# Kernel optimization log

Hardware: AMD Instinct MI355X
Metric: run time of the kernel (lower is better)

## Reference

```python
import jax, jax.numpy as jnp
import numpy as np
import math

D = 2048
H = 16
DH = D // H
DFF = 8192
B = 4
S = 2048
EPS = 1e-12


def gelu(x):
    # faithful tanh-approx gelu from source
    return 0.5 * x * (1.0 + jnp.tanh(math.sqrt(2.0 / math.pi) * (x + 0.044715 * x ** 3)))


def global_layernorm(x, w, b):
    # torch.mean(x)/torch.var(x): scalar mean and UNBIASED variance over ALL elements
    mean = jnp.mean(x)
    var = jnp.var(x, ddof=1)
    return (x - mean) / jnp.sqrt(var + EPS) * w + b


def setup_inputs() -> dict:
    key = jax.random.key(0)
    ks = jax.random.split(key, 12)
    sd = 0.02
    return {
        "x": jax.random.normal(ks[0], (B, S, D), jnp.float32),
        "W1_w": jax.random.normal(ks[1], (3 * D, D), jnp.float32) * sd,
        "W1_b": jnp.zeros((3 * D,), jnp.float32),
        "W2_w": jax.random.normal(ks[2], (D, D), jnp.float32) * sd,
        "W2_b": jnp.zeros((D,), jnp.float32),
        "fc_w": jax.random.normal(ks[3], (DFF, D), jnp.float32) * sd,
        "fc_b": jnp.zeros((DFF,), jnp.float32),
        "proj_w": jax.random.normal(ks[4], (D, DFF), jnp.float32) * sd,
        "proj_b": jnp.zeros((D,), jnp.float32),
        "ln1_w": jnp.ones((D,), jnp.float32),
        "ln1_b": jnp.zeros((D,), jnp.float32),
        "ln2_w": jnp.ones((D,), jnp.float32),
        "ln2_b": jnp.zeros((D,), jnp.float32),
    }


def attn(x, W1_w, W1_b, W2_w, W2_b):
    X = x @ W1_w.T + W1_b                     # [B,S,3D]
    Q, K, V = jnp.split(X, 3, axis=2)         # each [B,S,D]
    # reshape(): view (B,S,H,Dh) then permute
    q = Q.reshape(B, S, H, DH).transpose(0, 2, 3, 1)  # [B,H,Dh,S]
    k = K.reshape(B, S, H, DH).transpose(0, 2, 1, 3)  # [B,H,S,Dh]
    v = V.reshape(B, S, H, DH).transpose(0, 2, 3, 1)  # [B,H,Dh,S]
    # heads(): scores over head-feature dim, scaled by sqrt(q.size(-1)) = sqrt(S)
    w = jnp.einsum('bhds,bhse->bhde', q, k) / math.sqrt(S)  # [B,H,Dh,Dh]
    w = jax.nn.softmax(w, axis=-1)
    out = jnp.einsum('bhde,bhes->bhds', w, v)  # [B,H,Dh,S]
    # cat(): raw contiguous view [B,H,Dh,S] -> [B,S,H*Dh] (memory-order reshape)
    out = out.reshape(B, S, H * DH)
    return out @ W2_w.T + W2_b


def ffn(x, fc_w, fc_b, proj_w, proj_b):
    h = gelu(x @ fc_w.T + fc_b)
    return h @ proj_w.T + proj_b


def reference(x, W1_w, W1_b, W2_w, W2_b, fc_w, fc_b, proj_w, proj_b,
              ln1_w, ln1_b, ln2_w, ln2_b):
    a = attn(x, W1_w, W1_b, W2_w, W2_b)
    x = global_layernorm(a + x, ln1_w, ln1_b)
    m = ffn(x, fc_w, fc_b, proj_w, proj_b)
    x = global_layernorm(m + x, ln2_w, ln2_b)
    return x
```

## Files before the change

kernel.cpp:

```cpp
#include <hip/hip_runtime.h>
#include <math.h>

typedef float floatx4 __attribute__((ext_vector_type(4)));
typedef __bf16 bf16x8 __attribute__((ext_vector_type(8)));
typedef unsigned short ushortx8 __attribute__((ext_vector_type(8)));
typedef unsigned short ushortx4 __attribute__((ext_vector_type(4)));
typedef unsigned short ushortx2 __attribute__((ext_vector_type(2)));

typedef unsigned int __attribute__((address_space(1))) as1_uint;
typedef unsigned int __attribute__((address_space(3))) as3_uint;

#define DEV static __device__ __forceinline__

DEV unsigned short f32_bf16(float f) {
  unsigned u = __float_as_uint(f);
  u += 0x7FFFu + ((u >> 16) & 1u);
  return (unsigned short)(u >> 16);
}
DEV float bf16_f32(unsigned short h) { return __uint_as_float(((unsigned)h) << 16); }
DEV float gelu_f(float x) {
  float t2 = 1.5957691216057308f * (x + 0.044715f * x * x * x);
  return x * __builtin_amdgcn_rcpf(1.0f + __expf(-t2));
}
DEV void gload16(const void* g, void* l) {
  __builtin_amdgcn_global_load_lds((const as1_uint*)g, (as3_uint*)l, 16, 0, 0);
}
DEV floatx4 mfma16(ushortx8 a, ushortx8 b, floatx4 c) {
  return __builtin_amdgcn_mfma_f32_16x16x32_bf16(
      __builtin_bit_cast(bf16x8, a), __builtin_bit_cast(bf16x8, b), c, 0, 0, 0);
}


__global__ void zero_f(float* p, int n) {
  int i = threadIdx.x;
  if (i < n) p[i] = 0.f;
}

__global__ void cvt_f32_bf16(const float* __restrict__ in, unsigned short* __restrict__ out,
                             long n4) {
  long i = (long)blockIdx.x * blockDim.x + threadIdx.x;
  if (i >= n4) return;
  float4 v = ((const float4*)in)[i];
  ushortx4 o;
  o.x = f32_bf16(v.x); o.y = f32_bf16(v.y); o.z = f32_bf16(v.z); o.w = f32_bf16(v.w);
  ((ushortx4*)out)[i] = o;
}

__global__ void cvt_cols(const float* __restrict__ in, unsigned short* __restrict__ out,
                         int cbase, int cwlog4, long n4) {
  long i = (long)blockIdx.x * blockDim.x + threadIdx.x;
  if (i >= n4) return;
  int n = (int)(i >> cwlog4);
  int k4 = (int)(i & ((1 << cwlog4) - 1)) << 2;
  float4 v = *(const float4*)&in[(size_t)n * 8192 + cbase + k4];
  ushortx4 o;
  o.x = f32_bf16(v.x); o.y = f32_bf16(v.y); o.z = f32_bf16(v.z); o.w = f32_bf16(v.w);
  *(ushortx4*)&out[((size_t)n << (cwlog4 + 2)) + k4] = o;
}

__global__ __launch_bounds__(256) void softmax_k(const float* __restrict__ sc,
                                                 unsigned short* __restrict__ probs) {
  int r = blockIdx.x * 4 + (threadIdx.x >> 6);
  int lane = threadIdx.x & 63;
  size_t base = (size_t)(r >> 7) * 16384 + (size_t)(r & 127) * 128 + lane * 2;
  float2 p0 = *(const float2*)&sc[base];
  float2 p1 = *(const float2*)&sc[base + 1048576];
  float2 p2 = *(const float2*)&sc[base + 2097152];
  float2 p3 = *(const float2*)&sc[base + 3145728];
  const float scale = 0.022097086912079608f;
  float vx = (p0.x + p1.x + p2.x + p3.x) * scale;
  float vy = (p0.y + p1.y + p2.y + p3.y) * scale;
  float m = fmaxf(vx, vy);
#pragma unroll
  for (int off = 32; off; off >>= 1) m = fmaxf(m, __shfl_xor(m, off));
  float ex = expf(vx - m), ey = expf(vy - m);
  float s = ex + ey;
#pragma unroll
  for (int off = 32; off; off >>= 1) s += __shfl_xor(s, off);
  float inv = 1.f / s;
  ushortx2 o;
  o.x = f32_bf16(ex * inv);
  o.y = f32_bf16(ey * inv);
  *(ushortx2*)&probs[base] = o;
}

__global__ void ln_apply(const float* __restrict__ r, const float* __restrict__ stats,
                         const float* __restrict__ w, const float* __restrict__ bia,
                         float* __restrict__ outF, unsigned short* __restrict__ outB, long n4) {
  long i = (long)blockIdx.x * blockDim.x + threadIdx.x;
  if (i >= n4) return;
  const double total = 16777216.0;
  double mean = (double)stats[0] / total;
  double var = ((double)stats[1] - total * mean * mean) / (total - 1.0);
  float rstd = (float)(1.0 / sqrt(var + 1e-12));
  float fm = (float)mean;
  int col = (int)((i * 4) & 2047);
  float4 v = ((const float4*)r)[i];
  float4 wv = *(const float4*)&w[col];
  float4 bv = *(const float4*)&bia[col];
  float4 o;
  o.x = (v.x - fm) * rstd * wv.x + bv.x;
  o.y = (v.y - fm) * rstd * wv.y + bv.y;
  o.z = (v.z - fm) * rstd * wv.z + bv.z;
  o.w = (v.w - fm) * rstd * wv.w + bv.w;
  if (outF) ((float4*)outF)[i] = o;
  if (outB) {
    ushortx4 ob;
    ob.x = f32_bf16(o.x); ob.y = f32_bf16(o.y); ob.z = f32_bf16(o.z); ob.w = f32_bf16(o.w);
    ((ushortx4*)outB)[i] = ob;
  }
}

__global__ __launch_bounds__(256) void gemm_bt(
    const unsigned short* __restrict__ A, int lda, long sAo, long sAi,
    const unsigned short* __restrict__ B, int ldb, long sBo, long sBi,
    int K, int innerCnt,
    const float* __restrict__ bias, const float* __restrict__ residF,
    const unsigned short* __restrict__ residB, int accum,
    float* __restrict__ outF, unsigned short* __restrict__ outB,
    unsigned short* __restrict__ outQT,
    int ldc, long sCo, long sCi, int doGelu, float* __restrict__ stats) {
  __shared__ unsigned short As[128 * 64];
  __shared__ unsigned short Bs[128 * 64];
  const int tid = threadIdx.x;
  const int wave = tid >> 6;
  const int lane = tid & 63;
  const int z = blockIdx.z;
  const int zo = z / innerCnt, zi = z % innerCnt;
  const unsigned short* Ab = A + zo * sAo + zi * sAi;
  const unsigned short* Bb = B + zo * sBo + zi * sBi;
  const long coff = zo * sCo + zi * sCi;
  const int m0 = blockIdx.y * 128;
  const int n0 = blockIdx.x * 128;

  const int quad = lane >> 4;
  const int l16 = lane & 15;
  const int wm = (wave & 1) * 64;
  const int wn = (wave >> 1) * 64;
  const int srow = lane >> 3;
  const int kofs8 = (((lane & 7) ^ srow) & 7) * 8;

  floatx4 acc[4][4];
#pragma unroll
  for (int i = 0; i < 4; i++)
#pragma unroll
    for (int j = 0; j < 4; j++) acc[i][j] = (floatx4){0.f, 0.f, 0.f, 0.f};

  const int nK = K >> 6;
  for (int kt = 0; kt < nK; ++kt) {
    const int k0 = kt << 6;
    __syncthreads();
#pragma unroll
    for (int i = 0; i < 4; ++i) {
      const int rb = wave * 32 + i * 8;
      gload16(Ab + (size_t)(m0 + rb + srow) * lda + k0 + kofs8, &As[rb * 64]);
      gload16(Bb + (size_t)(n0 + rb + srow) * ldb + k0 + kofs8, &Bs[rb * 64]);
    }
    __syncthreads();
#pragma unroll
    for (int kk = 0; kk < 2; ++kk) {
      ushortx8 af[4], bf[4];
      const int swz = (l16 & 7);
#pragma unroll
      for (int i = 0; i < 4; i++)
        af[i] = *(const ushortx8*)&As[(wm + i * 16 + l16) * 64 +
                                      (((kk * 4 + quad) ^ swz) * 8)];
#pragma unroll
      for (int j = 0; j < 4; j++)
        bf[j] = *(const ushortx8*)&Bs[(wn + j * 16 + l16) * 64 +
                                      (((kk * 4 + quad) ^ swz) * 8)];
#pragma unroll
      for (int i = 0; i < 4; i++)
#pragma unroll
        for (int j = 0; j < 4; j++) acc[i][j] = mfma16(af[i], bf[j], acc[i][j]);
    }
  }

  float s1 = 0.f, s2 = 0.f;
#pragma unroll
  for (int i = 0; i < 4; i++) {
#pragma unroll
    for (int j = 0; j < 4; j++) {
      const int col = n0 + wn + j * 16 + l16;
      const float bv = bias ? bias[col] : 0.f;
#pragma unroll
      for (int r = 0; r < 4; r++) {
        const int row = m0 + wm + i * 16 + quad * 4 + r;
        float v = acc[i][j][r] + bv;
        if (doGelu) v = gelu_f(v);
        if (outQT) {
          const int b = row >> 11, s = row & 2047;
          if (col < 4096) {
            unsigned short* tb = outQT + ((col & 2048) ? 16777216u : 0u);
            const int cc = col & 2047;
            tb[((size_t)((b << 4) + (cc >> 7)) * 128 + (cc & 127)) * 2048 + s] = f32_bf16(v);
          } else {
            outB[(size_t)row * 2048 + (col - 4096)] = f32_bf16(v);
          }
          continue;
        }
        const size_t cidx = (size_t)coff + (size_t)row * ldc + col;
        if (residF) v += residF[cidx];
        if (residB) v += bf16_f32(residB[cidx]);
        if (accum) v += outF[cidx];
        if (outF) outF[cidx] = v;
        else outB[cidx] = f32_bf16(v);
        if (stats) { s1 += v; s2 += v * v; }
      }
    }
  }
  if (stats) {
#pragma unroll
    for (int off = 32; off; off >>= 1) {
      s1 += __shfl_down(s1, off);
      s2 += __shfl_down(s2, off);
    }
    if (lane == 0) {
      atomicAdd(&stats[0], s1);
      atomicAdd(&stats[1], s2);
    }
  }
}

__global__ __launch_bounds__(512, 2) void gemm256(
    const unsigned short* __restrict__ A, int lda,
    const unsigned short* __restrict__ B, int ldb, int K,
    const float* __restrict__ bias, const float* __restrict__ residF,
    const unsigned short* __restrict__ residB, int accum,
    float* __restrict__ outF, unsigned short* __restrict__ outB,
    unsigned short* __restrict__ outQT, int ldc, int doGelu,
    float* __restrict__ stats) {
  __shared__ unsigned short As0[256 * 64];
  __shared__ unsigned short As1[256 * 64];
  __shared__ unsigned short Bs0[256 * 64];
  __shared__ unsigned short Bs1[256 * 64];
  const int tid = threadIdx.x;
  const int wave = tid >> 6;
  const int lane = tid & 63;
  const int wm = wave >> 2;
  const int wn = wave & 3;
  const int quad = lane >> 4;
  const int l16 = lane & 15;
  const int swz = l16 & 7;

  const int nwg = gridDim.x * gridDim.y;
  const int orig = blockIdx.y * gridDim.x + blockIdx.x;
  const int q8 = nwg >> 3, r8 = nwg & 7;
  const int xcd = orig & 7, lid = orig >> 3;
  const int wgid = (xcd < r8 ? xcd * (q8 + 1) : r8 * (q8 + 1) + (xcd - r8) * q8) + lid;
  int m0, n0;
  if ((gridDim.x & 7) == 0) {
    const int gper = (int)(gridDim.y << 3);
    m0 = ((wgid % gper) >> 3) * 256;
    n0 = (((wgid / gper) << 3) + (wgid & 7)) * 256;
  } else {
    m0 = (wgid / gridDim.x) * 256;
    n0 = (wgid % gridDim.x) * 256;
  }

  const int srow = lane >> 3;
  const int kof = (((lane & 7) ^ srow) & 7) << 3;
  const int nkt = K >> 6;

  floatx4 acc[8][4];
#pragma unroll
  for (int i = 0; i < 8; i++)
#pragma unroll
    for (int j = 0; j < 4; j++) acc[i][j] = (floatx4){0.f, 0.f, 0.f, 0.f};

  auto stageB = [&](unsigned short* dst, int kt, int s) {
    const int k0 = kt << 6;
    const int rb = s * 128 + wave * 16;
    gload16(B + (size_t)(n0 + rb + srow) * ldb + k0 + kof, &dst[rb * 64]);
    gload16(B + (size_t)(n0 + rb + 8 + srow) * ldb + k0 + kof, &dst[(rb + 8) * 64]);
  };
  auto stageA = [&](unsigned short* dst, int kt, int hi) {
    const int k0 = kt << 6;
    const int rb = ((wave & 4) << 5) + ((wave & 3) << 4) + hi * 64;
    gload16(A + (size_t)(m0 + rb + srow) * lda + k0 + kof, &dst[rb * 64]);
    gload16(A + (size_t)(m0 + rb + 8 + srow) * lda + k0 + kof, &dst[(rb + 8) * 64]);
  };

  ushortx8 bfr[4][2], afr[2][2];
  const int aBase = (wm * 128 + l16) * 64;
  const int bBase = (wn * 64 + l16) * 64;
  const int kq0 = (quad ^ swz) << 3;
  const int kq1 = ((4 + quad) ^ swz) << 3;

  auto rdB = [&](const unsigned short* Bsb) {
#pragma unroll
    for (int fj = 0; fj < 4; fj++) {
      bfr[fj][0] = *(const ushortx8*)&Bsb[bBase + fj * 1024 + kq0];
      bfr[fj][1] = *(const ushortx8*)&Bsb[bBase + fj * 1024 + kq1];
    }
  };
  auto rdA = [&](const unsigned short* Asb, int p) {
#pragma unroll
    for (int fi = 0; fi < 2; fi++) {
      afr[fi][0] = *(const ushortx8*)&Asb[aBase + (p * 2 + fi) * 1024 + kq0];
      afr[fi][1] = *(const ushortx8*)&Asb[aBase + (p * 2 + fi) * 1024 + kq1];
    }
  };
  auto mma = [&](int p) {
    __builtin_amdgcn_s_setprio(1);
#pragma unroll
    for (int fi = 0; fi < 2; fi++)
#pragma unroll
      for (int fj = 0; fj < 4; fj++) {
        acc[p * 2 + fi][fj] = mfma16(afr[fi][0], bfr[fj][0], acc[p * 2 + fi][fj]);
        acc[p * 2 + fi][fj] = mfma16(afr[fi][1], bfr[fj][1], acc[p * 2 + fi][fj]);
      }
    __builtin_amdgcn_s_setprio(0);
  };

#define BAR() __builtin_amdgcn_s_barrier()
#define LGKM0()                                            \
  do {                                                     \
    asm volatile("s_waitcnt lgkmcnt(0)" ::: "memory");     \
    __builtin_amdgcn_sched_barrier(0);                     \
  } while (0)
#define LGKM8() asm volatile("s_waitcnt lgkmcnt(8)" ::: "memory")
#define VM6() asm volatile("s_waitcnt vmcnt(6)" ::: "memory")
#define VM0() asm volatile("s_waitcnt vmcnt(0)" ::: "memory")

  stageB(Bs0, 0, 0); stageB(Bs0, 0, 1); stageA(As0, 0, 0); stageA(As0, 0, 1);
  if (nkt > 1) { stageB(Bs1, 1, 0); stageB(Bs1, 1, 1); stageA(As1, 1, 0); }
  VM6();
  BAR();

  for (int kt = 0; kt < nkt; kt += 2) {
    const bool t2 = kt + 2 < nkt, t3 = kt + 3 < nkt;
    rdB(Bs0); rdA(As0, 0);
    if (kt + 1 < nkt) stageA(As1, kt + 1, 1);
    LGKM8();
    BAR(); LGKM0(); mma(0); BAR();

    rdA(As0, 1); if (t2) stageB(Bs0, kt + 2, 0);
    BAR(); LGKM0(); mma(1); BAR();

    rdA(As0, 2); if (t2) stageB(Bs0, kt + 2, 1);
    BAR(); LGKM0(); mma(2); BAR();

    rdA(As0, 3); if (t2) stageA(As0, kt + 2, 0);
    BAR(); LGKM0(); mma(3);
    if (t2) VM6(); else VM0();
    BAR();

    rdB(Bs1); rdA(As1, 0);
    if (t2) stageA(As0, kt + 2, 1);
    LGKM8();
    BAR(); LGKM0(); mma(0); BAR();

    rdA(As1, 1); if (t3) stageB(Bs1, kt + 3, 0);
    BAR(); LGKM0(); mma(1); BAR();

    rdA(As1, 2); if (t3) stageB(Bs1, kt + 3, 1);
    BAR(); LGKM0(); mma(2); BAR();

    rdA(As1, 3); if (t3) stageA(As1, kt + 3, 0);
    BAR(); LGKM0(); mma(3);
    if (t3) VM6();
    BAR();
  }
#undef BAR
#undef LGKM0
#undef LGKM8
#undef VM6
#undef VM0

  if (outQT) {
    if (n0 < 4096) {
      unsigned short* trb = (wave < 4) ? As0 + wave * 8192 : Bs0 + (wave - 4) * 8192;
#pragma unroll
      for (int j = 0; j < 4; j++) {
        const int c = j * 16 + l16;
        const float bv = bias ? bias[n0 + wn * 64 + c] : 0.f;
#pragma unroll
        for (int i = 0; i < 8; i++) {
          ushortx4 o;
          o.x = f32_bf16(acc[i][j][0] + bv);
          o.y = f32_bf16(acc[i][j][1] + bv);
          o.z = f32_bf16(acc[i][j][2] + bv);
          o.w = f32_bf16(acc[i][j][3] + bv);
          *(ushortx4*)&trb[c * 128 + (((i * 4 + quad) ^ (c & 6)) << 2)] = o;
        }
      }
      const int bb = m0 >> 11;
      const int sbase = (m0 & 2047) + wm * 128;
      unsigned short* tb = outQT + ((n0 & 2048) ? 16777216u : 0u);
      const int cg = lane >> 4;
      const int sl = lane & 15;
#pragma unroll
      for (int it = 0; it < 16; it++) {
        const int c = it * 4 + cg;
        ushortx8 v = *(const ushortx8*)&trb[c * 128 + (((2 * sl) ^ (c & 6)) << 2)];
        const int cc = (n0 + wn * 64 + c) & 2047;
        unsigned short* dst = tb +
            ((size_t)((bb << 4) + (cc >> 7)) * 128 + (cc & 127)) * 2048 + sbase + sl * 8;
        *(ushortx8*)dst = v;
      }
    } else {
#pragma unroll
      for (int i = 0; i < 8; i++)
#pragma unroll
        for (int j = 0; j < 4; j++) {
          const int col = n0 + wn * 64 + j * 16 + l16;
          const float bv = bias ? bias[col] : 0.f;
#pragma unroll
          for (int r = 0; r < 4; r++) {
            const int row = m0 + wm * 128 + i * 16 + quad * 4 + r;
            outB[(size_t)row * 2048 + (col - 4096)] = f32_bf16(acc[i][j][r] + bv);
          }
        }
    }
    return;
  }

  float s1 = 0.f, s2 = 0.f;
#pragma unroll
  for (int i = 0; i < 8; i++) {
#pragma unroll
    for (int j = 0; j < 4; j++) {
      const int col = n0 + wn * 64 + j * 16 + l16;
      const float bv = bias ? bias[col] : 0.f;
#pragma unroll
      for (int r = 0; r < 4; r++) {
        const int row = m0 + wm * 128 + i * 16 + quad * 4 + r;
        float v = acc[i][j][r] + bv;
        if (doGelu) v = gelu_f(v);
        const size_t cidx = (size_t)row * ldc + col;
        if (residF) v += residF[cidx];
        if (residB) v += bf16_f32(residB[cidx]);
        if (accum) v += outF[cidx];
        if (outF) outF[cidx] = v;
        else outB[cidx] = f32_bf16(v);
        if (stats) { s1 += v; s2 += v * v; }
      }
    }
  }
  if (stats) {
#pragma unroll
    for (int off = 32; off; off >>= 1) {
      s1 += __shfl_down(s1, off);
      s2 += __shfl_down(s2, off);
    }
    if (lane == 0) {
      atomicAdd(&stats[0], s1);
      atomicAdd(&stats[1], s2);
    }
  }
}


extern "C" void kernel_launch(void* const* d_in, const int* in_sizes, int n_in, void* d_out,
                              int out_size, void* d_ws, size_t ws_size, hipStream_t stream) {
  (void)in_sizes; (void)n_in; (void)out_size;
  const float* x    = (const float*)d_in[0];
  const float* W1w  = (const float*)d_in[1];
  const float* W1b  = (const float*)d_in[2];
  const float* W2w  = (const float*)d_in[3];
  const float* W2b  = (const float*)d_in[4];
  const float* fcw  = (const float*)d_in[5];
  const float* fcb  = (const float*)d_in[6];
  const float* pjw  = (const float*)d_in[7];
  const float* pjb  = (const float*)d_in[8];
  const float* ln1w = (const float*)d_in[9];
  const float* ln1b = (const float*)d_in[10];
  const float* ln2w = (const float*)d_in[11];
  const float* ln2b = (const float*)d_in[12];
  float* out = (float*)d_out;

  char* ws = (char*)d_ws;
  size_t off = 0;
  auto take = [&](size_t b) { size_t r = off; off = (off + b + 255) & ~(size_t)255; return r; };
  float* stats = (float*)(ws + take(256));
  size_t P0 = take(33554432);
  size_t P1 = take(25165824);
  size_t P2 = take(100663296);
  size_t P3 = off;

  unsigned short* xbf    = (unsigned short*)(ws + P0);
  unsigned short* attnbf = (unsigned short*)(ws + P0);
  unsigned short* W1bf   = (unsigned short*)(ws + P1);
  float*          spart  = (float*)(ws + P1);
  unsigned short* probs  = (unsigned short*)(ws + P1 + 16777216);
  unsigned short* W2bf   = (unsigned short*)(ws + P1);
  unsigned short* vbf    = (unsigned short*)(ws + P2);
  unsigned short* qT     = (unsigned short*)(ws + P2 + 33554432);
  float*          r12    = (float*)(ws + P2);
  unsigned short* x1bf   = (unsigned short*)(ws + P2 + 67108864);

  int nc;
  unsigned short *fc_ch, *pj_ch, *hch;
  if (ws_size >= P3 + 201326592) {
    nc = 1;
    fc_ch = (unsigned short*)(ws + P3);
    pj_ch = (unsigned short*)(ws + P3 + 33554432);
    hch   = (unsigned short*)(ws + P3 + 67108864);
  } else if (ws_size >= P3 + 100663296) {
    nc = 2;
    fc_ch = (unsigned short*)(ws + P3);
    pj_ch = (unsigned short*)(ws + P3 + 16777216);
    hch   = (unsigned short*)(ws + P3 + 33554432);
  } else {
    nc = 4;
    fc_ch = (unsigned short*)(ws + P1);
    pj_ch = (unsigned short*)(ws + P1 + 8388608);
    hch   = (unsigned short*)(ws + P0);
  }
  const int cw = 8192 / nc;
  const int cwlog4 = (nc == 1) ? 11 : (nc == 2) ? 10 : 9;
  const long cn4 = (long)cw << 9;

  zero_f<<<1, 64, 0, stream>>>(stats, 16);
  cvt_f32_bf16<<<16384, 256, 0, stream>>>(x, xbf, 4194304);
  cvt_f32_bf16<<<12288, 256, 0, stream>>>(W1w, W1bf, 3145728);

  gemm256<<<dim3(24, 32, 1), 512, 0, stream>>>(xbf, 2048, W1bf, 2048, 2048, W1b, nullptr,
                                               nullptr, 0, nullptr, vbf, qT, 0, 0, nullptr);
  gemm_bt<<<dim3(1, 1, 256), 256, 0, stream>>>(qT, 2048, 262144L, 512L, qT + 16777216, 2048,
                                               262144L, 512L, 512, 4, nullptr, nullptr, nullptr,
                                               0, spart, nullptr, nullptr, 128, 16384L, 1048576L,
                                               0, nullptr);
  softmax_k<<<2048, 256, 0, stream>>>(spart, probs);
  gemm_bt<<<dim3(16, 1, 64), 256, 0, stream>>>(probs, 128, 262144L, 16384L, vbf, 2048, 4194304L,
                                               128L, 128, 16, nullptr, nullptr, nullptr, 0,
                                               nullptr, attnbf, nullptr, 2048, 4194304L, 262144L,
                                               0, nullptr);
  cvt_f32_bf16<<<4096, 256, 0, stream>>>(W2w, W2bf, 1048576);
  gemm256<<<dim3(8, 32, 1), 512, 0, stream>>>(attnbf, 2048, W2bf, 2048, 2048, W2b, x, nullptr,
                                              0, r12, nullptr, nullptr, 2048, 0, stats);
  ln_apply<<<16384, 256, 0, stream>>>(r12, stats, ln1w, ln1b, nullptr, x1bf, 4194304);

  for (int c = 0; c < nc; ++c) {
    cvt_f32_bf16<<<(int)(cn4 / 256), 256, 0, stream>>>(fcw + (size_t)c * cw * 2048, fc_ch, cn4);
    cvt_cols<<<(int)(cn4 / 256), 256, 0, stream>>>(pjw, pj_ch, c * cw, cwlog4, cn4);
    gemm256<<<dim3(cw / 256, 32, 1), 512, 0, stream>>>(x1bf, 2048, fc_ch, 2048, 2048,
                                                       fcb + c * cw, nullptr, nullptr, 0,
                                                       nullptr, hch, nullptr, cw, 1, nullptr);
    const int last = (c == nc - 1);
    gemm256<<<dim3(8, 32, 1), 512, 0, stream>>>(hch, cw, pj_ch, cw, cw,
                                                last ? pjb : nullptr, nullptr,
                                                last ? x1bf : nullptr, c > 0, r12, nullptr,
                                                nullptr, 2048, 0,
                                                last ? (stats + 2) : nullptr);
  }
  ln_apply<<<16384, 256, 0, stream>>>(r12, stats + 2, ln2w, ln2b, out, nullptr, 4194304);
}
```

Baseline: 1.342 ms.

## Replace fine-grained interleaved GEMM pipeline with simple whole-tile double buffering

Replaces the hand-interleaved 8-phase K loop, with its many barriers and partial waitcnts, with a simpler scheme. Each K-tile loads all A/B fragments into registers up front, issues the global-to-LDS prefetch for the next tile, runs all 64 MFMAs, then waits on vmcnt(0) and a barrier. This removes most barriers but raises register pressure (16 A fragments held at once) and exposes more of the global load latency per tile. It also unconditionally stages kt+1 in the first half, which assumes an even number of K tiles.

```diff
diff --git a/kernel.cpp b/kernel.cpp
--- a/kernel.cpp
+++ b/kernel.cpp
@@ -268,105 +268,63 @@
 #pragma unroll
     for (int j = 0; j < 4; j++) acc[i][j] = (floatx4){0.f, 0.f, 0.f, 0.f};
 
-  auto stageB = [&](unsigned short* dst, int kt, int s) {
+  auto stageTile = [&](unsigned short* Aw, unsigned short* Bw, int kt) {
     const int k0 = kt << 6;
-    const int rb = s * 128 + wave * 16;
-    gload16(B + (size_t)(n0 + rb + srow) * ldb + k0 + kof, &dst[rb * 64]);
-    gload16(B + (size_t)(n0 + rb + 8 + srow) * ldb + k0 + kof, &dst[(rb + 8) * 64]);
+#pragma unroll
+    for (int s = 0; s < 2; s++) {
+      const int rb = s * 128 + wave * 16;
+      gload16(B + (size_t)(n0 + rb + srow) * ldb + k0 + kof, &Bw[rb * 64]);
+      gload16(B + (size_t)(n0 + rb + 8 + srow) * ldb + k0 + kof, &Bw[(rb + 8) * 64]);
+    }
+#pragma unroll
+    for (int hi = 0; hi < 2; hi++) {
+      const int rb = ((wave & 4) << 5) + ((wave & 3) << 4) + hi * 64;
+      gload16(A + (size_t)(m0 + rb + srow) * lda + k0 + kof, &Aw[rb * 64]);
+      gload16(A + (size_t)(m0 + rb + 8 + srow) * lda + k0 + kof, &Aw[(rb + 8) * 64]);
+    }
   };
-  auto stageA = [&](unsigned short* dst, int kt, int hi) {
-    const int k0 = kt << 6;
-    const int rb = ((wave & 4) << 5) + ((wave & 3) << 4) + hi * 64;
-    gload16(A + (size_t)(m0 + rb + srow) * lda + k0 + kof, &dst[rb * 64]);
-    gload16(A + (size_t)(m0 + rb + 8 + srow) * lda + k0 + kof, &dst[(rb + 8) * 64]);
-  };
-
-  ushortx8 bfr[4][2], afr[2][2];
+
   const int aBase = (wm * 128 + l16) * 64;
   const int bBase = (wn * 64 + l16) * 64;
   const int kq0 = (quad ^ swz) << 3;
   const int kq1 = ((4 + quad) ^ swz) << 3;
 
-  auto rdB = [&](const unsigned short* Bsb) {
+  auto tile = [&](const unsigned short* Ar, const unsigned short* Br,
+                  unsigned short* Aw, unsigned short* Bw, int ktNext, bool doStage) {
+    ushortx8 bfr[4][2], afr[8][2];
 #pragma unroll
     for (int fj = 0; fj < 4; fj++) {
-      bfr[fj][0] = *(const ushortx8*)&Bsb[bBase + fj * 1024 + kq0];
-      bfr[fj][1] = *(const ushortx8*)&Bsb[bBase + fj * 1024 + kq1];
-    }
-  };
-  auto rdA = [&](const unsigned short* Asb, int p) {
-#pragma unroll
-    for (int fi = 0; fi < 2; fi++) {
-      afr[fi][0] = *(const ushortx8*)&Asb[aBase + (p * 2 + fi) * 1024 + kq0];
-      afr[fi][1] = *(const ushortx8*)&Asb[aBase + (p * 2 + fi) * 1024 + kq1];
-    }
-  };
-  auto mma = [&](int p) {
+      bfr[fj][0] = *(const ushortx8*)&Br[bBase + fj * 1024 + kq0];
+      bfr[fj][1] = *(const ushortx8*)&Br[bBase + fj * 1024 + kq1];
+    }
+#pragma unroll
+    for (int m = 0; m < 8; m++) {
+      afr[m][0] = *(const ushortx8*)&Ar[aBase + m * 1024 + kq0];
+      afr[m][1] = *(const ushortx8*)&Ar[aBase + m * 1024 + kq1];
+    }
+    __builtin_amdgcn_sched_barrier(0);
+    if (doStage) stageTile(Aw, Bw, ktNext);
     __builtin_amdgcn_s_setprio(1);
 #pragma unroll
-    for (int fi = 0; fi < 2; fi++)
-#pragma unroll
-      for (int fj = 0; fj < 4; fj++) {
-        acc[p * 2 + fi][fj] = mfma16(afr[fi][0], bfr[fj][0], acc[p * 2 + fi][fj]);
-        acc[p * 2 + fi][fj] = mfma16(afr[fi][1], bfr[fj][1], acc[p * 2 + fi][fj]);
+    for (int m = 0; m < 8; m++)
+#pragma unroll
+      for (int n = 0; n < 4; n++) {
+        acc[m][n] = mfma16(afr[m][0], bfr[n][0], acc[m][n]);
+        acc[m][n] = mfma16(afr[m][1], bfr[n][1], acc[m][n]);
       }
     __builtin_amdgcn_s_setprio(0);
+    asm volatile("s_waitcnt vmcnt(0)" ::: "memory");
+    __builtin_amdgcn_s_barrier();
   };
 
-#define BAR() __builtin_amdgcn_s_barrier()
-#define LGKM0()                                            \
-  do {                                                     \
-    asm volatile("s_waitcnt lgkmcnt(0)" ::: "memory");     \
-    __builtin_amdgcn_sched_barrier(0);                     \
-  } while (0)
-#define LGKM8() asm volatile("s_waitcnt lgkmcnt(8)" ::: "memory")
-#define VM6() asm volatile("s_waitcnt vmcnt(6)" ::: "memory")
-#define VM0() asm volatile("s_waitcnt vmcnt(0)" ::: "memory")
-
-  stageB(Bs0, 0, 0); stageB(Bs0, 0, 1); stageA(As0, 0, 0); stageA(As0, 0, 1);
-  if (nkt > 1) { stageB(Bs1, 1, 0); stageB(Bs1, 1, 1); stageA(As1, 1, 0); }
-  VM6();
-  BAR();
+  stageTile(As0, Bs0, 0);
+  asm volatile("s_waitcnt vmcnt(0)" ::: "memory");
+  __builtin_amdgcn_s_barrier();
 
   for (int kt = 0; kt < nkt; kt += 2) {
-    const bool t2 = kt + 2 < nkt, t3 = kt + 3 < nkt;
-    rdB(Bs0); rdA(As0, 0);
-    if (kt + 1 < nkt) stageA(As1, kt + 1, 1);
-    LGKM8();
-    BAR(); LGKM0(); mma(0); BAR();
-
-    rdA(As0, 1); if (t2) stageB(Bs0, kt + 2, 0);
-    BAR(); LGKM0(); mma(1); BAR();
-
-    rdA(As0, 2); if (t2) stageB(Bs0, kt + 2, 1);
-    BAR(); LGKM0(); mma(2); BAR();
-
-    rdA(As0, 3); if (t2) stageA(As0, kt + 2, 0);
-    BAR(); LGKM0(); mma(3);
-    if (t2) VM6(); else VM0();
-    BAR();
-
-    rdB(Bs1); rdA(As1, 0);
-    if (t2) stageA(As0, kt + 2, 1);
-    LGKM8();
-    BAR(); LGKM0(); mma(0); BAR();
-
-    rdA(As1, 1); if (t3) stageB(Bs1, kt + 3, 0);
-    BAR(); LGKM0(); mma(1); BAR();
-
-    rdA(As1, 2); if (t3) stageB(Bs1, kt + 3, 1);
-    BAR(); LGKM0(); mma(2); BAR();
-
-    rdA(As1, 3); if (t3) stageA(As1, kt + 3, 0);
-    BAR(); LGKM0(); mma(3);
-    if (t3) VM6();
-    BAR();
-  }
-#undef BAR
-#undef LGKM0
-#undef LGKM8
-#undef VM6
-#undef VM0
+    tile(As0, Bs0, As1, Bs1, kt + 1, true);
+    tile(As1, Bs1, As0, Bs0, kt + 2, kt + 2 < nkt);
+  }
 
   if (outQT) {
     if (n0 < 4096) {
```

After: 1.781 ms. +32.7%, slower.
